# Kernel tuning notes

Hardware: AMD Instinct MI355X
Metric: run time of the kernel (lower is better)

Reference implementation:

```python
import jax, jax.numpy as jnp
import numpy as np

HEAD, DIM, R = 8, 256, 3
RA = (2 * R + 1) ** 2  # 49


def conv2d(x, w, b=None, pad=0, groups=1):
    y = jax.lax.conv_general_dilated(x, w, (1, 1), [(pad, pad), (pad, pad)],
                                     dimension_numbers=('NCHW', 'OIHW', 'NCHW'),
                                     feature_group_count=groups)
    return y if b is None else y + b[None, :, None, None]


def grid_sample(img, grid, mode, padding='zeros'):
    # img [B,C,H,W]; grid [B,Hg,Wg,2] with (x,y) in [-1,1]; align_corners=False.
    B, C, H, W = img.shape
    Hg, Wg = grid.shape[1], grid.shape[2]
    gx = ((grid[..., 0] + 1.0) * W - 1.0) / 2.0
    gy = ((grid[..., 1] + 1.0) * H - 1.0) / 2.0
    if padding == 'border':
        gx = jnp.clip(gx, 0.0, W - 1.0)
        gy = jnp.clip(gy, 0.0, H - 1.0)
    gx = gx.reshape(B, -1)
    gy = gy.reshape(B, -1)

    def gather(iy, ix):
        iyc = jnp.clip(iy, 0, H - 1)
        ixc = jnp.clip(ix, 0, W - 1)
        return jax.vmap(lambda im, a, b: im[:, a, b])(img, iyc, ixc)  # [B,C,N]

    def mask(iy, ix):
        if padding == 'border':
            return jnp.ones(iy.shape, img.dtype)
        return ((ix >= 0) & (ix < W) & (iy >= 0) & (iy < H)).astype(img.dtype)

    if mode == 'nearest':
        ix = jnp.round(gx).astype(jnp.int32)
        iy = jnp.round(gy).astype(jnp.int32)
        out = gather(iy, ix) * mask(iy, ix)[:, None, :]
    else:  # bilinear
        x0f = jnp.floor(gx); y0f = jnp.floor(gy)
        wx = gx - x0f; wy = gy - y0f
        x0 = x0f.astype(jnp.int32); y0 = y0f.astype(jnp.int32)
        out = jnp.zeros((B, C, gx.shape[1]), img.dtype)
        for dx, dy, w in ((0, 0, (1 - wx) * (1 - wy)), (1, 0, wx * (1 - wy)),
                          (0, 1, (1 - wx) * wy), (1, 1, wx * wy)):
            ix = x0 + dx; iy = y0 + dy
            out = out + gather(iy, ix) * (w * mask(iy, ix))[:, None, :]
    return out.reshape(B, C, Hg, Wg)


def mlp2(x, W1, b1, W2, b2):
    return jax.nn.relu(x @ W1.T + b1) @ W2.T + b2


def setup_inputs() -> dict:
    key = jax.random.key(0)
    ks = jax.random.split(key, 32)
    B, H, W, Q = 1, 64, 64, 4096
    f32 = jnp.float32
    rn = lambda k, shp, s=0.02: jax.random.normal(k, shp, f32) * s
    return {
        'inp': jax.random.normal(ks[0], (B, 3, H, W), f32),
        'coord': jax.random.uniform(ks[1], (B, Q, 2), f32, -1.0, 1.0),
        'cell': jnp.full((B, Q, 2), 2.0 / (2 * H), f32),
        'W_enc': rn(ks[2], (64, 3, 3, 3)), 'b_enc': jnp.zeros((64,), f32),
        'W_ch': rn(ks[3], (256, 64, 3, 3)), 'b_ch': jnp.zeros((256,), f32),
        'W_q': rn(ks[4], (256, 256, 3, 3)), 'b_q': jnp.zeros((256,), f32),
        'W_k': rn(ks[5], (256, 256, 3, 3)), 'b_k': jnp.zeros((256,), f32),
        'W_v': rn(ks[6], (256, 256, 3, 3)), 'b_v': jnp.zeros((256,), f32),
        'W_off1': rn(ks[7], (256, 32, 5, 5)), 'b_off1': jnp.zeros((256,), f32),
        'ln_g': jnp.ones((256,), f32), 'ln_b': jnp.zeros((256,), f32),
        'W_off2': rn(ks[8], (98, 256, 1, 1)),
        'Wc1': rn(ks[9], (256, 98)), 'bc1': jnp.zeros((256,), f32),
        'Wc2': rn(ks[10], (49, 256)), 'bc2': jnp.zeros((49,), f32),
        'Wi1': rn(ks[11], (256, 12546)), 'bi1': jnp.zeros((256,), f32),
        'Wi2': rn(ks[12], (3, 256)), 'bi2': jnp.zeros((3,), f32),
        'scale': 2,
    }


def reference(inp, coord, cell, W_enc, b_enc, W_ch, b_ch, W_q, b_q, W_k, b_k,
              W_v, b_v, W_off1, b_off1, ln_g, ln_b, W_off2, Wc1, bc1, Wc2, bc2,
              Wi1, bi1, Wi2, bi2, scale):
    B, _, H, W = inp.shape
    Q = coord.shape[1]
    # gen_feat: encoder stub (conv+relu) -> conv_ch -> q/k/v convs
    feat = conv2d(jax.nn.relu(conv2d(inp, W_enc, b_enc, pad=1)), W_ch, b_ch, pad=1)
    fq = conv2d(feat, W_q, b_q, pad=1)
    fk = conv2d(feat, W_k, b_k, pad=1)
    fv = conv2d(feat, W_v, b_v, pad=1)
    # offset branch: grouped 5x5 conv -> channelwise LN -> GELU -> 1x1 conv (no bias)
    o = conv2d(feat, W_off1, b_off1, pad=2, groups=8)
    oc = o.transpose(0, 2, 3, 1)
    mu = oc.mean(-1, keepdims=True)
    var = ((oc - mu) ** 2).mean(-1, keepdims=True)
    oc = (oc - mu) / jnp.sqrt(var + 1e-5) * ln_g + ln_b
    offsets = conv2d(jax.nn.gelu(oc.transpose(0, 3, 1, 2), approximate=False), W_off2, None, pad=0)  # [B,98,H,W]
    # LR coordinate grid (y,x) at pixel centers in [-1,1]
    ys = -1.0 + 1.0 / H + (2.0 / H) * jnp.arange(H, dtype=inp.dtype)
    xs = -1.0 + 1.0 / W + (2.0 / W) * jnp.arange(W, dtype=inp.dtype)
    coord_lr = jnp.broadcast_to(jnp.stack(jnp.meshgrid(ys, xs, indexing='ij'), 0)[None], (B, 2, H, W))
    sc = coord[:, :, None, :]          # [B,Q,1,2] (y,x)
    g = sc[..., ::-1]                  # (x,y) for grid_sample
    sck = grid_sample(coord_lr, g, 'nearest').transpose(0, 2, 3, 1)  # [B,Q,1,2]
    off = grid_sample(offsets, g, 'nearest').transpose(0, 2, 3, 1).reshape(B, Q, RA, 2)
    off = jnp.tanh(off) * jnp.array([1.0 / (H - 1.0), 1.0 / (W - 1.0)], inp.dtype) * 2.0
    d = jnp.linspace(-R, R, 2 * R + 1).astype(inp.dtype)
    delta = jnp.stack(jnp.meshgrid(d * (2.0 / H), d * (2.0 / W), indexing='ij'), -1).reshape(1, 1, RA, 2)
    sck = sck + delta + off            # [B,Q,49,2] sampling locs (y,x)
    q = grid_sample(fq, g, 'bilinear').transpose(0, 2, 3, 1).reshape(B, Q, HEAD, DIM // HEAD)
    k = grid_sample(fk, sck[..., ::-1], 'nearest').transpose(0, 2, 3, 1).reshape(B, Q, RA, HEAD, DIM // HEAD)
    v = grid_sample(fv, sck[..., ::-1], 'nearest').transpose(0, 2, 3, 1).reshape(B, Q, RA, HEAD, DIM // HEAD)
    attn_val = jnp.einsum('bqhd,bqkhd->bqkh', q, k) / np.sqrt(DIM // HEAD)  # [B,Q,49,8]
    rel = (sc - sck) * jnp.array([H, W], inp.dtype)  # [B,Q,49,2]
    wcoord = mlp2(rel.reshape(B * Q, RA * 2), Wc1, bc1, Wc2, bc2).reshape(B, Q, RA, 1)
    attn = jax.nn.softmax(wcoord + attn_val, axis=2)  # softmax over 49 samples
    feat_in = (v * attn[..., None]).reshape(B, Q, RA * DIM)
    rel_cell = cell * jnp.array([H, W], inp.dtype)
    feat_in = jnp.concatenate([feat_in, rel_cell], -1)  # [B,Q,12546]
    pred = mlp2(feat_in.reshape(B * Q, -1), Wi1, bi1, Wi2, bi2).reshape(B, Q, 3)
    skip = grid_sample(inp, g, 'bilinear', 'border')[:, :, :, 0].transpose(0, 2, 1)
    return pred + skip
```

## Files before the change

kernel.cpp:

```cpp
#include <hip/hip_runtime.h>
#include <hip/hip_bf16.h>


typedef unsigned short u16;
typedef unsigned int u32;
using frag_ab = __attribute__((ext_vector_type(8))) short;
using frag_cd = __attribute__((ext_vector_type(4))) float;

#define HW 4096
#define NQ 4096
#define KBIG 12576
#define SPLITK 16
#define KCHUNK 800
#define KQ 2304
#define QSPLIT 3
#define QCHUNK 768
#define NBLK_QKV (64 * 6 * QSPLIT)
#define NBLK_OFF1 (64 * 8)

static __device__ __forceinline__ u16 f2b(float f) {
  union { __hip_bfloat16 h; u16 u; } c; c.h = __float2bfloat16(f); return c.u;
}
static __device__ __forceinline__ float b2f(u16 v) {
  return __uint_as_float((u32)v << 16);
}
static __device__ __forceinline__ u32 pk2(float a, float b) {
  union { __hip_bfloat162 h; u32 u; } c;
  c.h = __float22bfloat162_rn(float2{a, b});
  return c.u;
}
static __device__ __forceinline__ void glds16(const u16* g, u16* l) {
  __builtin_amdgcn_global_load_lds(
      (const __attribute__((address_space(1))) u32*)(g),
      (__attribute__((address_space(3))) u32*)(l), 16, 0, 0);
}

#define BM 64
#define BN 64
#define BK 32
#define LDSS 40

__global__ __launch_bounds__(256)
void gemm_bt(const u16* __restrict__ A, const u16* __restrict__ Bt,
             void* __restrict__ Cv, const float* __restrict__ bias,
             int N, int K, int ldc, int flags,
             long sA, long sB, long sC, int sBias)
{
  __shared__ u16 As[BM * LDSS];
  __shared__ u16 Bs[BN * LDSS];
  const int z = blockIdx.z;
  A  += (long)z * sA;
  Bt += (long)z * sB;
  const float* bz = bias ? bias + (long)z * sBias : nullptr;

  const int tid  = threadIdx.x;
  const int m0   = blockIdx.x * BM;
  const int n0   = blockIdx.y * BN;
  const int wave = tid >> 6, lane = tid & 63;
  const int mw = (wave & 1) * 32, nw = (wave >> 1) * 32;
  const int lr = lane & 15, lk = lane >> 4;
  const int srow = tid >> 2, scol = (tid & 3) * 8;

  frag_cd acc[2][2] = {};
  const u16* aptr = A + (size_t)(m0 + srow) * K + scol;
  const bool bok  = (n0 + srow) < N;
  const u16* bptr = Bt + (size_t)(n0 + srow) * K + scol;

  uint4 av = *(const uint4*)(aptr);
  uint4 bv = bok ? *(const uint4*)(bptr) : uint4{0u, 0u, 0u, 0u};

  for (int k0 = 0; k0 < K; k0 += BK) {
    *(uint4*)&As[srow * LDSS + scol] = av;
    *(uint4*)&Bs[srow * LDSS + scol] = bv;
    __syncthreads();
    if (k0 + BK < K) {
      av = *(const uint4*)(aptr + k0 + BK);
      bv = bok ? *(const uint4*)(bptr + k0 + BK) : uint4{0u, 0u, 0u, 0u};
    }
    frag_ab af0 = *(const frag_ab*)&As[(mw      + lr) * LDSS + lk * 8];
    frag_ab af1 = *(const frag_ab*)&As[(mw + 16 + lr) * LDSS + lk * 8];
    frag_ab bf0 = *(const frag_ab*)&Bs[(nw      + lr) * LDSS + lk * 8];
    frag_ab bf1 = *(const frag_ab*)&Bs[(nw + 16 + lr) * LDSS + lk * 8];
    acc[0][0] = __builtin_amdgcn_mfma_f32_16x16x32_bf16(af0, bf0, acc[0][0], 0, 0, 0);
    acc[0][1] = __builtin_amdgcn_mfma_f32_16x16x32_bf16(af0, bf1, acc[0][1], 0, 0, 0);
    acc[1][0] = __builtin_amdgcn_mfma_f32_16x16x32_bf16(af1, bf0, acc[1][0], 0, 0, 0);
    acc[1][1] = __builtin_amdgcn_mfma_f32_16x16x32_bf16(af1, bf1, acc[1][1], 0, 0, 0);
    __syncthreads();
  }

  const bool relu = flags & 1;
  const bool obf  = flags & 2;
  #pragma unroll
  for (int i = 0; i < 2; i++)
    #pragma unroll
    for (int j = 0; j < 2; j++) {
      int col = n0 + nw + j * 16 + lr;
      if (col >= N) continue;
      float badd = bz ? bz[col] : 0.f;
      #pragma unroll
      for (int r = 0; r < 4; r++) {
        int row = m0 + mw + i * 16 + lk * 4 + r;
        float v = acc[i][j][r] + badd;
        if (relu) v = fmaxf(v, 0.f);
        size_t idx = (size_t)z * sC + (size_t)row * ldc + col;
        if (obf) ((u16*)Cv)[idx] = f2b(v);
        else     ((float*)Cv)[idx] = v;
      }
    }
}

template<int W3, int SH, int PAD>
__global__ __launch_bounds__(256)
void gemm_conv(const u16* __restrict__ feat, const u16* __restrict__ Bt,
               void* __restrict__ Cv, const float* __restrict__ bias,
               int N, int K, int ldc, int flags, int FC, int cbStride,
               long sB, long sC, int sBias)
{
  __shared__ u16 As[BM * LDSS];
  __shared__ u16 Bs[BN * LDSS];
  const int z = blockIdx.z;
  Bt += (long)z * sB;
  const float* bz = bias ? bias + (long)z * sBias : nullptr;
  const int cb = z * cbStride;

  const int tid  = threadIdx.x;
  const int m0   = blockIdx.x * BM;
  const int n0   = blockIdx.y * BN;
  const int wave = tid >> 6, lane = tid & 63;
  const int mw = (wave & 1) * 32, nw = (wave >> 1) * 32;
  const int lr = lane & 15, lk = lane >> 4;
  const int srow = tid >> 2, scol = (tid & 3) * 8;
  const int p = m0 + srow, y = p >> 6, x = p & 63;

  frag_cd acc[2][2] = {};
  const bool bok  = (n0 + srow) < N;
  const u16* bptr = Bt + (size_t)(n0 + srow) * K + scol;

  auto stageA = [&](int k0) -> uint4 {
    int k = k0 + scol;
    int s = k >> SH;
    int c = k & ((1 << SH) - 1);
    int dy = s / W3, dx = s - dy * W3;
    int yy = y + dy - PAD, xx = x + dx - PAD;
    if (((unsigned)yy < 64u) && ((unsigned)xx < 64u))
      return *(const uint4*)&feat[(size_t)(yy * 64 + xx) * FC + cb + c];
    return uint4{0u, 0u, 0u, 0u};
  };

  uint4 av = stageA(0);
  uint4 bv = bok ? *(const uint4*)(bptr) : uint4{0u, 0u, 0u, 0u};

  for (int k0 = 0; k0 < K; k0 += BK) {
    *(uint4*)&As[srow * LDSS + scol] = av;
    *(uint4*)&Bs[srow * LDSS + scol] = bv;
    __syncthreads();
    if (k0 + BK < K) {
      av = stageA(k0 + BK);
      bv = bok ? *(const uint4*)(bptr + k0 + BK) : uint4{0u, 0u, 0u, 0u};
    }
    frag_ab af0 = *(const frag_ab*)&As[(mw      + lr) * LDSS + lk * 8];
    frag_ab af1 = *(const frag_ab*)&As[(mw + 16 + lr) * LDSS + lk * 8];
    frag_ab bf0 = *(const frag_ab*)&Bs[(nw      + lr) * LDSS + lk * 8];
    frag_ab bf1 = *(const frag_ab*)&Bs[(nw + 16 + lr) * LDSS + lk * 8];
    acc[0][0] = __builtin_amdgcn_mfma_f32_16x16x32_bf16(af0, bf0, acc[0][0], 0, 0, 0);
    acc[0][1] = __builtin_amdgcn_mfma_f32_16x16x32_bf16(af0, bf1, acc[0][1], 0, 0, 0);
    acc[1][0] = __builtin_amdgcn_mfma_f32_16x16x32_bf16(af1, bf0, acc[1][0], 0, 0, 0);
    acc[1][1] = __builtin_amdgcn_mfma_f32_16x16x32_bf16(af1, bf1, acc[1][1], 0, 0, 0);
    __syncthreads();
  }

  const bool relu = flags & 1;
  const bool obf  = flags & 2;
  #pragma unroll
  for (int i = 0; i < 2; i++)
    #pragma unroll
    for (int j = 0; j < 2; j++) {
      int col = n0 + nw + j * 16 + lr;
      if (col >= N) continue;
      float badd = bz ? bz[col] : 0.f;
      #pragma unroll
      for (int r = 0; r < 4; r++) {
        int row = m0 + mw + i * 16 + lk * 4 + r;
        float v = acc[i][j][r] + badd;
        if (relu) v = fmaxf(v, 0.f);
        size_t idx = (size_t)z * sC + (size_t)row * ldc + col;
        if (obf) ((u16*)Cv)[idx] = f2b(v);
        else     ((float*)Cv)[idx] = v;
      }
    }
}

__global__ __launch_bounds__(256)
void gemm_feat(const u16* __restrict__ feat, const u16* __restrict__ Btqkv,
               u16* __restrict__ Pq, const u16* __restrict__ Btoff1,
               float* __restrict__ obuf, const float* __restrict__ b_off1)
{
  __shared__ u16 smem[6656];
  const int bid = blockIdx.x;
  const int tid = threadIdx.x;
  const int wave = tid >> 6, lane = tid & 63;
  const int lr = lane & 15, lk = lane >> 4;

  if (bid < NBLK_QKV) {
    u16* As = smem;
    u16* Bs = smem + 64 * 40;
    const int mz  = bid & 63;
    const int rest = bid >> 6;
    const int ny  = rest % 6;
    const int z   = rest / 6;
    const int m0  = mz * 64;
    const int n0  = ny * 128;
    const int kbeg = z * QCHUNK;
    const int kend = kbeg + QCHUNK;
    const int nw = wave * 32;
    const int arow = tid >> 2, acol = (tid & 3) * 8;
    const int p = m0 + arow, y = p >> 6, x = p & 63;

    frag_cd acc[4][2] = {};
    const u16* bbase = Btqkv + (size_t)(n0 + (tid >> 2)) * KQ + (tid & 3) * 8 + kbeg;
    u16* bdst = &Bs[(size_t)tid * 8];

    auto stageA = [&](int k0) -> uint4 {
      int k = k0 + acol;
      int s = k >> 8, c = k & 255;
      int dy = s / 3, dx = s - dy * 3;
      int yy = y + dy - 1, xx = x + dx - 1;
      if (((unsigned)yy < 64u) && ((unsigned)xx < 64u))
        return *(const uint4*)&feat[(size_t)(yy * 64 + xx) * 256 + c];
      return uint4{0u, 0u, 0u, 0u};
    };

    uint4 av = stageA(kbeg);

    for (int k0 = kbeg; k0 < kend; k0 += BK) {
      glds16(bbase + (k0 - kbeg), bdst);
      glds16(bbase + (k0 - kbeg) + (size_t)64 * KQ, bdst + 2048);
      *(uint4*)&As[arow * LDSS + acol] = av;
      __syncthreads();
      if (k0 + BK < kend) av = stageA(k0 + BK);
      frag_ab af[4];
      #pragma unroll
      for (int i = 0; i < 4; i++)
        af[i] = *(const frag_ab*)&As[(i * 16 + lr) * LDSS + lk * 8];
      #pragma unroll
      for (int j = 0; j < 2; j++) {
        frag_ab bf = *(const frag_ab*)&Bs[(nw + j * 16 + lr) * 32 + lk * 8];
        #pragma unroll
        for (int i = 0; i < 4; i++)
          acc[i][j] = __builtin_amdgcn_mfma_f32_16x16x32_bf16(af[i], bf, acc[i][j], 0, 0, 0);
      }
      __syncthreads();
    }

    #pragma unroll
    for (int i = 0; i < 4; i++)
      #pragma unroll
      for (int j = 0; j < 2; j++) {
        int col = n0 + nw + j * 16 + lr;
        #pragma unroll
        for (int r = 0; r < 4; r++) {
          int row = m0 + i * 16 + lk * 4 + r;
          Pq[(size_t)z * (NQ * 768) + (size_t)row * 768 + col] = f2b(acc[i][j][r]);
        }
      }
  } else {
    u16* As = smem;
    u16* Bs = smem + 64 * 40;
    const int t  = bid - NBLK_QKV;
    const int m0 = (t & 63) * 64;
    const int g  = t >> 6;
    const int cb = g * 32;
    const u16* Bt = Btoff1 + (size_t)g * 32 * 800;
    const float* bz = b_off1 + g * 32;
    const int mw = (wave & 1) * 32, nw = (wave >> 1) * 32;
    const int srow = tid >> 2, scol = (tid & 3) * 8;
    const int p = m0 + srow, y = p >> 6, x = p & 63;

    frag_cd acc[2][2] = {};
    const bool bok  = srow < 32;
    const u16* bptr = Bt + (size_t)srow * 800 + scol;

    auto stageA = [&](int k0) -> uint4 {
      int k = k0 + scol;
      int s = k >> 5;
      int c = k & 31;
      int dy = s / 5, dx = s - dy * 5;
      int yy = y + dy - 2, xx = x + dx - 2;
      if (((unsigned)yy < 64u) && ((unsigned)xx < 64u))
        return *(const uint4*)&feat[(size_t)(yy * 64 + xx) * 256 + cb + c];
      return uint4{0u, 0u, 0u, 0u};
    };

    uint4 av = stageA(0);
    uint4 bv = bok ? *(const uint4*)(bptr) : uint4{0u, 0u, 0u, 0u};

    for (int k0 = 0; k0 < 800; k0 += BK) {
      *(uint4*)&As[srow * LDSS + scol] = av;
      *(uint4*)&Bs[srow * LDSS + scol] = bv;
      __syncthreads();
      if (k0 + BK < 800) {
        av = stageA(k0 + BK);
        bv = bok ? *(const uint4*)(bptr + k0 + BK) : uint4{0u, 0u, 0u, 0u};
      }
      frag_ab af0 = *(const frag_ab*)&As[(mw      + lr) * LDSS + lk * 8];
      frag_ab af1 = *(const frag_ab*)&As[(mw + 16 + lr) * LDSS + lk * 8];
      frag_ab bf0 = *(const frag_ab*)&Bs[(nw      + lr) * LDSS + lk * 8];
      frag_ab bf1 = *(const frag_ab*)&Bs[(nw + 16 + lr) * LDSS + lk * 8];
      acc[0][0] = __builtin_amdgcn_mfma_f32_16x16x32_bf16(af0, bf0, acc[0][0], 0, 0, 0);
      acc[0][1] = __builtin_amdgcn_mfma_f32_16x16x32_bf16(af0, bf1, acc[0][1], 0, 0, 0);
      acc[1][0] = __builtin_amdgcn_mfma_f32_16x16x32_bf16(af1, bf0, acc[1][0], 0, 0, 0);
      acc[1][1] = __builtin_amdgcn_mfma_f32_16x16x32_bf16(af1, bf1, acc[1][1], 0, 0, 0);
      __syncthreads();
    }

    #pragma unroll
    for (int i = 0; i < 2; i++)
      #pragma unroll
      for (int j = 0; j < 2; j++) {
        int col = nw + j * 16 + lr;
        if (col >= 32) continue;
        float badd = bz[col];
        #pragma unroll
        for (int r = 0; r < 4; r++) {
          int row = m0 + mw + i * 16 + lk * 4 + r;
          obuf[(size_t)row * 256 + g * 32 + col] = acc[i][j][r] + badd;
        }
      }
  }
}

__global__ __launch_bounds__(256)
void reduce_qkv(const u16* __restrict__ P, const float* __restrict__ bias,
                u16* __restrict__ outb, float* __restrict__ outV)
{
  int i8 = blockIdx.x * 256 + threadIdx.x;
  if (i8 >= NQ * 96) return;
  size_t i = (size_t)i8 * 8;
  int row = (int)(i / 768);
  int c = (int)(i % 768);
  float v[8];
  #pragma unroll
  for (int t = 0; t < 8; t++) v[t] = bias[c + t];
  for (int z = 0; z < QSPLIT; z++) {
    uint4 a = *(const uint4*)&P[(size_t)z * (NQ * 768) + i];
    u32 aw[4] = {a.x, a.y, a.z, a.w};
    #pragma unroll
    for (int t = 0; t < 4; t++) {
      v[2 * t]     += __uint_as_float(aw[t] << 16);
      v[2 * t + 1] += __uint_as_float(aw[t] & 0xffff0000u);
    }
  }
  uint4 ob = {pk2(v[0], v[1]), pk2(v[2], v[3]), pk2(v[4], v[5]), pk2(v[6], v[7])};
  *(uint4*)&outb[i] = ob;
  if (c >= 512) {
    float* dst = outV + (size_t)row * 256 + (c - 512);
    *(float4*)dst       = float4{v[0], v[1], v[2], v[3]};
    *(float4*)(dst + 4) = float4{v[4], v[5], v[6], v[7]};
  }
}

__global__ __launch_bounds__(512, 4)
void gemm_big(const u16* __restrict__ Bt, const float* __restrict__ fqkvV,
              const float* __restrict__ attnval, const int* __restrict__ vidx,
              const float* __restrict__ cell, u16* __restrict__ P)
{
  __shared__ u16 As[128 * LDSS];
  __shared__ u16 Bs[256 * 32];
  __shared__ int   s_vidx[5 * 128];
  __shared__ float s_attn[5 * 128 * 8];
  const int tid  = threadIdx.x;
  const int m0   = blockIdx.x * 128;
  const int z    = blockIdx.y;
  const int kbeg = z * KCHUNK;
  const int kend = min(KBIG, kbeg + KCHUNK);
  const int jbeg = kbeg >> 8;
  const int jcnt = ((kend - 1) >> 8) - jbeg + 1;
  const int wave = tid >> 6, lane = tid & 63;
  const int mw = (wave & 1) * 64, nwv = (wave >> 1) * 64;
  const int lr = lane & 15, lk = lane >> 4;
  const int arow = tid >> 2, acol = (tid & 3) * 8;
  const int q = m0 + arow;

  for (int t = tid; t < 128 * jcnt; t += 512) {
    int r = t & 127, jj = t >> 7;
    int j = jbeg + jj;
    s_vidx[t] = (j < 49) ? vidx[(m0 + r) * 49 + j] : -1;
  }
  for (int t = tid; t < 128 * 8 * jcnt; t += 512) {
    int h = t & 7, rr = (t >> 3) & 127, jj = t >> 10;
    int j = jbeg + jj;
    s_attn[t] = (j < 49) ? attnval[((size_t)((m0 + rr) * 49 + j)) * 8 + h] : 0.f;
  }
  __syncthreads();

  auto loadA = [&](int k0, float4& f0, float4& f1, float& w) {
    const int k = k0 + acol;
    const int j = k >> 8, c = k & 255;
    f0 = float4{0.f, 0.f, 0.f, 0.f};
    f1 = float4{0.f, 0.f, 0.f, 0.f};
    w = 0.f;
    if (j < 49) {
      const int jj = j - jbeg;
      int id = s_vidx[jj * 128 + arow];
      if (id >= 0) {
        w = s_attn[(jj * 128 + arow) * 8 + (c >> 5)];
        const float* src = fqkvV + (size_t)id * 256 + c;
        f0 = *(const float4*)src;
        f1 = *(const float4*)(src + 4);
      }
    } else if (c == 0) {
      f0.x = cell[q * 2]; f0.y = cell[q * 2 + 1];
      w = 64.f;
    }
  };

  frag_cd acc[4][4] = {};
  float4 f0c, f1c; float wc_;
  loadA(kbeg, f0c, f1c, wc_);
  const u16* bbase = Bt + (size_t)(tid >> 2) * KBIG + (tid & 3) * 8 + kbeg;
  u16* bdst = &Bs[(size_t)tid * 8];

  for (int k0 = kbeg; k0 < kend; k0 += BK) {
    glds16(bbase + (k0 - kbeg), bdst);
    glds16(bbase + (k0 - kbeg) + (size_t)128 * KBIG, bdst + 4096);
    {
      uint4 av;
      av.x = pk2(f0c.x * wc_, f0c.y * wc_);
      av.y = pk2(f0c.z * wc_, f0c.w * wc_);
      av.z = pk2(f1c.x * wc_, f1c.y * wc_);
      av.w = pk2(f1c.z * wc_, f1c.w * wc_);
      *(uint4*)&As[arow * LDSS + acol] = av;
    }
    __syncthreads();
    if (k0 + BK < kend) loadA(k0 + BK, f0c, f1c, wc_);
    frag_ab af[4];
    #pragma unroll
    for (int i = 0; i < 4; i++)
      af[i] = *(const frag_ab*)&As[(mw + i * 16 + lr) * LDSS + lk * 8];
    #pragma unroll
    for (int j = 0; j < 4; j++) {
      frag_ab bf = *(const frag_ab*)&Bs[(nwv + j * 16 + lr) * 32 + lk * 8];
      #pragma unroll
      for (int i = 0; i < 4; i++)
        acc[i][j] = __builtin_amdgcn_mfma_f32_16x16x32_bf16(af[i], bf, acc[i][j], 0, 0, 0);
    }
    __syncthreads();
  }

  #pragma unroll
  for (int i = 0; i < 4; i++)
    #pragma unroll
    for (int j = 0; j < 4; j++) {
      int col = nwv + j * 16 + lr;
      #pragma unroll
      for (int r = 0; r < 4; r++) {
        int row = m0 + mw + i * 16 + lk * 4 + r;
        P[(size_t)z * (NQ * 256) + (size_t)row * 256 + col] = f2b(acc[i][j][r]);
      }
    }
}

__global__ __launch_bounds__(256)
void reduce_final(const u16* __restrict__ Pb, const float* __restrict__ bi1,
                  const float* __restrict__ Wi2, const float* __restrict__ bi2,
                  const float* __restrict__ skipb, float* __restrict__ out)
{
  const int q = blockIdx.x, c = threadIdx.x;
  float s = 0.f;
  #pragma unroll
  for (int z = 0; z < SPLITK; z++)
    s += b2f(Pb[(size_t)z * (NQ * 256) + (size_t)q * 256 + c]);
  s += bi1[c];
  s = fmaxf(s, 0.f);

  __shared__ float part[3][4];
  float p0 = s * Wi2[c], p1 = s * Wi2[256 + c], p2 = s * Wi2[512 + c];
  #pragma unroll
  for (int off = 32; off; off >>= 1) {
    p0 += __shfl_xor(p0, off);
    p1 += __shfl_xor(p1, off);
    p2 += __shfl_xor(p2, off);
  }
  if ((c & 63) == 0) {
    int w = c >> 6;
    part[0][w] = p0; part[1][w] = p1; part[2][w] = p2;
  }
  __syncthreads();
  if (c < 3)
    out[q * 3 + c] = bi2[c] + skipb[q * 3 + c]
                   + part[c][0] + part[c][1] + part[c][2] + part[c][3];
}

__global__ __launch_bounds__(512)
void softmax_k(const float* __restrict__ wc, float* __restrict__ attnval)
{
  const int q = blockIdx.x;
  const int tid = threadIdx.x;
  const int hh = tid >> 6, l = tid & 63;
  float v = (l < 49) ? wc[(size_t)q * 49 + l] + attnval[((size_t)q * 49 + l) * 8 + hh]
                     : -1e30f;
  float m = v;
  #pragma unroll
  for (int off = 32; off; off >>= 1) m = fmaxf(m, __shfl_xor(m, off));
  float e = (l < 49) ? expf(v - m) : 0.f;
  float s = e;
  #pragma unroll
  for (int off = 32; off; off >>= 1) s += __shfl_xor(s, off);
  if (l < 49) attnval[((size_t)q * 49 + l) * 8 + hh] = e / s;
}

static __device__ __forceinline__
void packconv(const float* __restrict__ W, u16* __restrict__ Bt,
              int Cin, int K2, int idx)
{
  int o  = idx / (Cin * K2);
  int r  = idx - o * (Cin * K2);
  int ci = r / K2;
  int s  = r - ci * K2;
  Bt[(size_t)o * (Cin * K2) + s * Cin + ci] = f2b(W[idx]);
}
static __device__ __forceinline__
void packcast(const float* __restrict__ W, u16* __restrict__ Bt,
              int Kin, int Kout, int idx)
{
  int n = idx / Kout, k = idx - n * Kout;
  Bt[idx] = f2b(k < Kin ? W[(size_t)n * Kin + k] : 0.f);
}

#define SZ_CH   147456
#define SZ_QKV  589824
#define SZ_OFF1 204800
#define SZ_OFF2 25088
#define SZ_C1   32768
#define SZ_C2   12544
#define SZ_WI1  3219456
#define SZ_PACK (SZ_CH + 3*SZ_QKV + SZ_OFF1 + SZ_OFF2 + SZ_C1 + SZ_C2 + 768 + SZ_WI1)

__global__ void pack_all(const float* W_ch, const float* W_q, const float* W_k,
                         const float* W_v, const float* W_off1, const float* W_off2,
                         const float* Wc1, const float* Wc2, const float* Wi1,
                         const float* b_q, const float* b_k, const float* b_v,
                         u16* Btch, u16* Btqkv, u16* Btoff1, u16* Btoff2,
                         u16* Btc1, u16* Btc2, u16* Wi1p, float* bqkv)
{
  int i = blockIdx.x * 256 + threadIdx.x;
  if (i < SZ_CH) { packconv(W_ch, Btch, 64, 9, i); return; }
  i -= SZ_CH;
  if (i < SZ_QKV) { packconv(W_q, Btqkv, 256, 9, i); return; }
  i -= SZ_QKV;
  if (i < SZ_QKV) { packconv(W_k, Btqkv + (size_t)256 * 2304, 256, 9, i); return; }
  i -= SZ_QKV;
  if (i < SZ_QKV) { packconv(W_v, Btqkv + (size_t)512 * 2304, 256, 9, i); return; }
  i -= SZ_QKV;
  if (i < SZ_OFF1) { packconv(W_off1, Btoff1, 32, 25, i); return; }
  i -= SZ_OFF1;
  if (i < SZ_OFF2) { packcast(W_off2, Btoff2, 256, 256, i); return; }
  i -= SZ_OFF2;
  if (i < SZ_C1) { packcast(Wc1, Btc1, 98, 128, i); return; }
  i -= SZ_C1;
  if (i < SZ_C2) { packcast(Wc2, Btc2, 256, 256, i); return; }
  i -= SZ_C2;
  if (i < 768) {
    bqkv[i] = (i < 256) ? b_q[i] : (i < 512) ? b_k[i - 256] : b_v[i - 512];
    return;
  }
  i -= 768;
  if (i < SZ_WI1) { packcast(Wi1, Wi1p, 12546, 12576, i); }
}

__global__ __launch_bounds__(64)
void conv_enc(const float* __restrict__ inp, const float* __restrict__ W,
              const float* __restrict__ b, u16* __restrict__ feat1)
{
  const int p = blockIdx.x, c = threadIdx.x;
  const int y = p >> 6, x = p & 63;
  float s = b[c];
  #pragma unroll
  for (int ci = 0; ci < 3; ci++)
    #pragma unroll
    for (int dy = 0; dy < 3; dy++) {
      int yy = y + dy - 1;
      if ((unsigned)yy >= 64u) continue;
      #pragma unroll
      for (int dx = 0; dx < 3; dx++) {
        int xx = x + dx - 1;
        if ((unsigned)xx >= 64u) continue;
        s += inp[ci * HW + yy * 64 + xx] * W[((c * 3 + ci) * 3 + dy) * 3 + dx];
      }
    }
  feat1[(size_t)p * 64 + c] = f2b(fmaxf(s, 0.f));
}

__global__ __launch_bounds__(256)
void ln_gelu(const float* __restrict__ x, const float* __restrict__ g,
             const float* __restrict__ b, u16* __restrict__ y)
{
  const int p = blockIdx.x, c = threadIdx.x;
  __shared__ float r1[4], r2[4];
  float v = x[(size_t)p * 256 + c];
  float s1 = v, s2 = v * v;
  #pragma unroll
  for (int off = 32; off; off >>= 1) {
    s1 += __shfl_xor(s1, off);
    s2 += __shfl_xor(s2, off);
  }
  if ((c & 63) == 0) { r1[c >> 6] = s1; r2[c >> 6] = s2; }
  __syncthreads();
  float t1 = r1[0] + r1[1] + r1[2] + r1[3];
  float t2 = r2[0] + r2[1] + r2[2] + r2[3];
  float mu  = t1 * (1.f / 256.f);
  float var = t2 * (1.f / 256.f) - mu * mu;
  float xn = (v - mu) * rsqrtf(var + 1e-5f) * g[c] + b[c];
  float ge = 0.5f * xn * (1.f + erff(xn * 0.70710678118654752f));
  y[(size_t)p * 256 + c] = f2b(ge);
}

__global__ __launch_bounds__(256)
void sampler(const float* __restrict__ coord, const u16* __restrict__ fqkvb,
             const float* __restrict__ offs, const float* __restrict__ inp,
             float* __restrict__ attnval, u16* __restrict__ relbuf,
             int* __restrict__ vidx, float* __restrict__ skipb)
{
  const int q = blockIdx.x;
  const int tid = threadIdx.x;
  __shared__ float s_off[98];
  __shared__ int s_idx[49];
  __shared__ float s_q[256];

  const float c0 = coord[q * 2], c1 = coord[q * 2 + 1];
  const float gxp = ((c1 + 1.f) * 64.f - 1.f) * 0.5f;
  const float gyp = ((c0 + 1.f) * 64.f - 1.f) * 0.5f;
  const int ixn = (int)rintf(gxp), iyn = (int)rintf(gyp);
  const bool inn = ((unsigned)ixn < 64u) && ((unsigned)iyn < 64u);

  if (tid < 98) {
    float v = inn ? offs[(size_t)(iyn * 64 + ixn) * 98 + tid] : 0.f;
    s_off[tid] = tanhf(v) * (2.f / 63.f);
  }
  __syncthreads();

  const float scky = inn ? (-1.f + (float)(2 * iyn + 1) * (1.f / 64.f)) : 0.f;
  const float sckx = inn ? (-1.f + (float)(2 * ixn + 1) * (1.f / 64.f)) : 0.f;

  if (tid < 49) {
    const int a = tid / 7, bb = tid - a * 7;
    float sy = scky + (float)(a - 3) * (2.f / 64.f) + s_off[2 * tid];
    float sx = sckx + (float)(bb - 3) * (2.f / 64.f) + s_off[2 * tid + 1];
    relbuf[(size_t)q * 128 + 2 * tid]     = f2b((c0 - sy) * 64.f);
    relbuf[(size_t)q * 128 + 2 * tid + 1] = f2b((c1 - sx) * 64.f);
    float gx2 = ((sx + 1.f) * 64.f - 1.f) * 0.5f;
    float gy2 = ((sy + 1.f) * 64.f - 1.f) * 0.5f;
    int ix2 = (int)rintf(gx2), iy2 = (int)rintf(gy2);
    int id = (((unsigned)ix2 < 64u) && ((unsigned)iy2 < 64u)) ? (iy2 * 64 + ix2) : -1;
    s_idx[tid] = id;
    vidx[q * 49 + tid] = id;
  } else if (tid >= 98 && tid < 128) {
    relbuf[(size_t)q * 128 + tid] = 0;
  }

  {
    const float x0f = floorf(gxp), y0f = floorf(gyp);
    const float wx = gxp - x0f, wy = gyp - y0f;
    const int x0 = (int)x0f, y0 = (int)y0f;
    float qc = 0.f;
    #pragma unroll
    for (int t = 0; t < 4; t++) {
      int xi = x0 + (t & 1), yi = y0 + (t >> 1);
      if (((unsigned)xi < 64u) && ((unsigned)yi < 64u)) {
        float w = ((t & 1) ? wx : 1.f - wx) * ((t >> 1) ? wy : 1.f - wy);
        qc += w * b2f(fqkvb[(size_t)(yi * 64 + xi) * 768 + tid]);
      }
    }
    s_q[tid] = qc * 0.17677669529663687f;
  }

  if (tid < 3) {
    float gx = fminf(fmaxf(gxp, 0.f), 63.f);
    float gy = fminf(fmaxf(gyp, 0.f), 63.f);
    float xf = floorf(gx), yf = floorf(gy);
    float wxs = gx - xf, wys = gy - yf;
    int xa = (int)xf, ya = (int)yf;
    int xb = min(xa + 1, 63), yb = min(ya + 1, 63);
    const float* ch = inp + tid * HW;
    float v = (1.f - wxs) * (1.f - wys) * ch[ya * 64 + xa]
            + wxs * (1.f - wys) * ch[ya * 64 + xb]
            + (1.f - wxs) * wys * ch[yb * 64 + xa]
            + wxs * wys * ch[yb * 64 + xb];
    skipb[q * 3 + tid] = v;
  }
  __syncthreads();

  const int wave = tid >> 6, lane = tid & 63;
  const int half = lane >> 5, sub = lane & 31;
  const int ch0 = sub * 8;
  const int h = sub >> 2;
  float qv[8];
  #pragma unroll
  for (int i = 0; i < 8; i++) qv[i] = s_q[ch0 + i];

  for (int it = 0; it < 7; it++) {
    int j = it * 8 + wave * 2 + half;
    if (j >= 49) break;
    int id = s_idx[j];
    float p = 0.f;
    if (id >= 0) {
      uint4 kv = *(const uint4*)&fqkvb[(size_t)id * 768 + 256 + ch0];
      u32 w0 = kv.x, w1 = kv.y, w2 = kv.z, w3 = kv.w;
      p = fmaf(qv[0], __uint_as_float(w0 << 16), p);
      p = fmaf(qv[1], __uint_as_float(w0 & 0xffff0000u), p);
      p = fmaf(qv[2], __uint_as_float(w1 << 16), p);
      p = fmaf(qv[3], __uint_as_float(w1 & 0xffff0000u), p);
      p = fmaf(qv[4], __uint_as_float(w2 << 16), p);
      p = fmaf(qv[5], __uint_as_float(w2 & 0xffff0000u), p);
      p = fmaf(qv[6], __uint_as_float(w3 << 16), p);
      p = fmaf(qv[7], __uint_as_float(w3 & 0xffff0000u), p);
    }
    p += __shfl_down(p, 2, 4);
    p += __shfl_down(p, 1, 4);
    if ((sub & 3) == 0) attnval[((size_t)q * 49 + j) * 8 + h] = p;
  }
}

extern "C" void kernel_launch(void* const* d_in, const int* in_sizes, int n_in,
                              void* d_out, int out_size, void* d_ws, size_t ws_size,
                              hipStream_t stream)
{
  const float* inp    = (const float*)d_in[0];
  const float* coord  = (const float*)d_in[1];
  const float* cell   = (const float*)d_in[2];
  const float* W_enc  = (const float*)d_in[3];
  const float* b_enc  = (const float*)d_in[4];
  const float* W_ch   = (const float*)d_in[5];
  const float* b_ch   = (const float*)d_in[6];
  const float* W_q    = (const float*)d_in[7];
  const float* b_q    = (const float*)d_in[8];
  const float* W_k    = (const float*)d_in[9];
  const float* b_k    = (const float*)d_in[10];
  const float* W_v    = (const float*)d_in[11];
  const float* b_v    = (const float*)d_in[12];
  const float* W_off1 = (const float*)d_in[13];
  const float* b_off1 = (const float*)d_in[14];
  const float* ln_g   = (const float*)d_in[15];
  const float* ln_b   = (const float*)d_in[16];
  const float* W_off2 = (const float*)d_in[17];
  const float* Wc1    = (const float*)d_in[18];
  const float* bc1    = (const float*)d_in[19];
  const float* Wc2    = (const float*)d_in[20];
  const float* bc2    = (const float*)d_in[21];
  const float* Wi1    = (const float*)d_in[22];
  const float* bi1    = (const float*)d_in[23];
  const float* Wi2    = (const float*)d_in[24];
  const float* bi2    = (const float*)d_in[25];

  char* base = (char*)d_ws;
  size_t off = 0;
  auto alloc = [&](size_t bytes) -> char* {
    char* r = base + off;
    off = (off + bytes + 255) & ~(size_t)255;
    return r;
  };

  float* obuf   = (float*)alloc((size_t)HW * 256 * 4);
  u16*   ocg    = (u16*)  alloc((size_t)HW * 256 * 2);
  float* offsb  = (float*)alloc((size_t)HW * 98 * 4);
  u16*   feat1  = (u16*)  alloc((size_t)HW * 64 * 2);
  u16*   feat   = (u16*)  alloc((size_t)HW * 256 * 2);
  u16*   hid1   = (u16*)  alloc((size_t)NQ * 256 * 2);
  float* wcb    = (float*)alloc((size_t)NQ * 49 * 4);
  u16*   relbuf = (u16*)  alloc((size_t)NQ * 128 * 2);
  u16*   Btqkv  = (u16*)  alloc((size_t)768 * 2304 * 2);
  u16*   Btch   = (u16*)  alloc((size_t)256 * 576 * 2);
  u16*   Btoff1 = (u16*)  alloc((size_t)256 * 800 * 2);
  u16*   Btoff2 = (u16*)  alloc((size_t)98 * 256 * 2);
  u16*   Btc1   = (u16*)  alloc((size_t)256 * 128 * 2);
  u16*   Btc2   = (u16*)  alloc((size_t)49 * 256 * 2);
  u16* Pb = (u16*)base;
  u16* Pqb = (u16*)(base + ((size_t)36 << 20));
  {
    size_t need = ((size_t)36 << 20) + (size_t)QSPLIT * NQ * 768 * 2;
    if (off < need) off = (need + 255) & ~(size_t)255;
  }
  u16*   fqkvb   = (u16*)  alloc((size_t)HW * 768 * 2);
  float* fqkvV   = (float*)alloc((size_t)HW * 256 * 4);
  float* attnval = (float*)alloc((size_t)NQ * 49 * 8 * 4);
  int*   vidxb   = (int*)  alloc((size_t)NQ * 49 * 4);
  float* skipb   = (float*)alloc((size_t)NQ * 3 * 4);
  u16*   Wi1p    = (u16*)  alloc((size_t)256 * KBIG * 2);
  float* bqkv    = (float*)alloc(768 * 4);
  (void)ws_size; (void)in_sizes; (void)n_in; (void)out_size;

  pack_all<<<(SZ_PACK + 255) / 256, 256, 0, stream>>>(
      W_ch, W_q, W_k, W_v, W_off1, W_off2, Wc1, Wc2, Wi1, b_q, b_k, b_v,
      Btch, Btqkv, Btoff1, Btoff2, Btc1, Btc2, Wi1p, bqkv);

  conv_enc<<<HW, 64, 0, stream>>>(inp, W_enc, b_enc, feat1);
  gemm_conv<3, 6, 1><<<dim3(64, 4, 1), 256, 0, stream>>>(
      feat1, Btch, feat, b_ch, 256, 576, 256, 2, 64, 0, 0, 0, 0);
  gemm_feat<<<NBLK_QKV + NBLK_OFF1, 256, 0, stream>>>(
      feat, Btqkv, Pqb, Btoff1, obuf, b_off1);
  reduce_qkv<<<(NQ * 96 + 255) / 256, 256, 0, stream>>>(Pqb, bqkv, fqkvb, fqkvV);
  ln_gelu<<<HW, 256, 0, stream>>>(obuf, ln_g, ln_b, ocg);
  gemm_bt<<<dim3(64, 2, 1), 256, 0, stream>>>(ocg, Btoff2, offsb, nullptr,
      98, 256, 98, 0, 0, 0, 0, 0);

  sampler<<<NQ, 256, 0, stream>>>(coord, fqkvb, offsb, inp,
                                  attnval, relbuf, vidxb, skipb);
  gemm_bt<<<dim3(64, 4, 1), 256, 0, stream>>>(relbuf, Btc1, hid1, bc1,
      256, 128, 256, 3, 0, 0, 0, 0);
  gemm_bt<<<dim3(64, 1, 1), 256, 0, stream>>>(hid1, Btc2, wcb, bc2,
      49, 256, 49, 0, 0, 0, 0, 0);
  softmax_k<<<NQ, 512, 0, stream>>>(wcb, attnval);

  gemm_big<<<dim3(32, SPLITK), 512, 0, stream>>>(
      Wi1p, fqkvV, attnval, vidxb, cell, Pb);
  reduce_final<<<NQ, 256, 0, stream>>>(Pb, bi1, Wi2, bi2, skipb, (float*)d_out);
}
```

Measured before the change: 288.5 us.

## Store V features in bf16 for gathers and retune big GEMM split-K

reduce_qkv now writes the V slice as packed bf16 instead of fp32. gemm_big gathers 16-byte bf16 rows and unpacks them before scaling by the attention weight, which halves the bytes moved by the irregular V gather. The big GEMM also goes from 16 to 24 split-K slices with a smaller K chunk. The shared index and attention staging arrays shrink to 3 j-slots and launch bounds ask for 6 blocks per CU, aiming for more parallelism and occupancy. The cost is an extra bf16 rounding of V before the multiply and more partial sums written and reduced.

```diff
diff --git a/kernel.cpp b/kernel.cpp
--- a/kernel.cpp
+++ b/kernel.cpp
@@ -10,8 +10,9 @@
 #define HW 4096
 #define NQ 4096
 #define KBIG 12576
-#define SPLITK 16
-#define KCHUNK 800
+#define SPLITK 24
+#define KCHUNK 544
+#define JMAX 3
 #define KQ 2304
 #define QSPLIT 3
 #define QCHUNK 768
@@ -331,7 +332,7 @@
 
 __global__ __launch_bounds__(256)
 void reduce_qkv(const u16* __restrict__ P, const float* __restrict__ bias,
-                u16* __restrict__ outb, float* __restrict__ outV)
+                u16* __restrict__ outb, u16* __restrict__ outV)
 {
   int i8 = blockIdx.x * 256 + threadIdx.x;
   if (i8 >= NQ * 96) return;
@@ -353,21 +354,19 @@
   uint4 ob = {pk2(v[0], v[1]), pk2(v[2], v[3]), pk2(v[4], v[5]), pk2(v[6], v[7])};
   *(uint4*)&outb[i] = ob;
   if (c >= 512) {
-    float* dst = outV + (size_t)row * 256 + (c - 512);
-    *(float4*)dst       = float4{v[0], v[1], v[2], v[3]};
-    *(float4*)(dst + 4) = float4{v[4], v[5], v[6], v[7]};
-  }
-}
-
-__global__ __launch_bounds__(512, 4)
-void gemm_big(const u16* __restrict__ Bt, const float* __restrict__ fqkvV,
+    *(uint4*)&outV[(size_t)row * 256 + (c - 512)] = ob;
+  }
+}
+
+__global__ __launch_bounds__(512, 6)
+void gemm_big(const u16* __restrict__ Bt, const u16* __restrict__ fqkvV,
               const float* __restrict__ attnval, const int* __restrict__ vidx,
               const float* __restrict__ cell, u16* __restrict__ P)
 {
   __shared__ u16 As[128 * LDSS];
   __shared__ u16 Bs[256 * 32];
-  __shared__ int   s_vidx[5 * 128];
-  __shared__ float s_attn[5 * 128 * 8];
+  __shared__ int   s_vidx[JMAX * 128];
+  __shared__ float s_attn[JMAX * 128 * 8];
   const int tid  = threadIdx.x;
   const int m0   = blockIdx.x * 128;
   const int z    = blockIdx.y;
@@ -393,30 +392,27 @@
   }
   __syncthreads();
 
-  auto loadA = [&](int k0, float4& f0, float4& f1, float& w) {
+  auto loadA = [&](int k0, uint4& kv, float& w) {
     const int k = k0 + acol;
     const int j = k >> 8, c = k & 255;
-    f0 = float4{0.f, 0.f, 0.f, 0.f};
-    f1 = float4{0.f, 0.f, 0.f, 0.f};
+    kv = uint4{0u, 0u, 0u, 0u};
     w = 0.f;
     if (j < 49) {
       const int jj = j - jbeg;
       int id = s_vidx[jj * 128 + arow];
       if (id >= 0) {
         w = s_attn[(jj * 128 + arow) * 8 + (c >> 5)];
-        const float* src = fqkvV + (size_t)id * 256 + c;
-        f0 = *(const float4*)src;
-        f1 = *(const float4*)(src + 4);
+        kv = *(const uint4*)(fqkvV + (size_t)id * 256 + c);
       }
     } else if (c == 0) {
-      f0.x = cell[q * 2]; f0.y = cell[q * 2 + 1];
+      kv.x = pk2(cell[q * 2], cell[q * 2 + 1]);
       w = 64.f;
     }
   };
 
   frag_cd acc[4][4] = {};
-  float4 f0c, f1c; float wc_;
-  loadA(kbeg, f0c, f1c, wc_);
+  uint4 kvc; float wc_;
+  loadA(kbeg, kvc, wc_);
   const u16* bbase = Bt + (size_t)(tid >> 2) * KBIG + (tid & 3) * 8 + kbeg;
   u16* bdst = &Bs[(size_t)tid * 8];
 
@@ -424,15 +420,20 @@
     glds16(bbase + (k0 - kbeg), bdst);
     glds16(bbase + (k0 - kbeg) + (size_t)128 * KBIG, bdst + 4096);
     {
+      u32 aw[4] = {kvc.x, kvc.y, kvc.z, kvc.w};
       uint4 av;
-      av.x = pk2(f0c.x * wc_, f0c.y * wc_);
-      av.y = pk2(f0c.z * wc_, f0c.w * wc_);
-      av.z = pk2(f1c.x * wc_, f1c.y * wc_);
-      av.w = pk2(f1c.z * wc_, f1c.w * wc_);
+      u32 avw[4];
+      #pragma unroll
+      for (int t = 0; t < 4; t++) {
+        float lo = __uint_as_float(aw[t] << 16) * wc_;
+        float hi = __uint_as_float(aw[t] & 0xffff0000u) * wc_;
+        avw[t] = pk2(lo, hi);
+      }
+      av.x = avw[0]; av.y = avw[1]; av.z = avw[2]; av.w = avw[3];
       *(uint4*)&As[arow * LDSS + acol] = av;
     }
     __syncthreads();
-    if (k0 + BK < kend) loadA(k0 + BK, f0c, f1c, wc_);
+    if (k0 + BK < kend) loadA(k0 + BK, kvc, wc_);
     frag_ab af[4];
     #pragma unroll
     for (int i = 0; i < 4; i++)
@@ -781,7 +782,7 @@
     if (off < need) off = (need + 255) & ~(size_t)255;
   }
   u16*   fqkvb   = (u16*)  alloc((size_t)HW * 768 * 2);
-  float* fqkvV   = (float*)alloc((size_t)HW * 256 * 4);
+  u16*   fqkvVb  = (u16*)  alloc((size_t)HW * 256 * 2);
   float* attnval = (float*)alloc((size_t)NQ * 49 * 8 * 4);
   int*   vidxb   = (int*)  alloc((size_t)NQ * 49 * 4);
   float* skipb   = (float*)alloc((size_t)NQ * 3 * 4);
@@ -798,7 +799,7 @@
       feat1, Btch, feat, b_ch, 256, 576, 256, 2, 64, 0, 0, 0, 0);
   gemm_feat<<<NBLK_QKV + NBLK_OFF1, 256, 0, stream>>>(
       feat, Btqkv, Pqb, Btoff1, obuf, b_off1);
-  reduce_qkv<<<(NQ * 96 + 255) / 256, 256, 0, stream>>>(Pqb, bqkv, fqkvb, fqkvV);
+  reduce_qkv<<<(NQ * 96 + 255) / 256, 256, 0, stream>>>(Pqb, bqkv, fqkvb, fqkvVb);
   ln_gelu<<<HW, 256, 0, stream>>>(obuf, ln_g, ln_b, ocg);
   gemm_bt<<<dim3(64, 2, 1), 256, 0, stream>>>(ocg, Btoff2, offsb, nullptr,
       98, 256, 98, 0, 0, 0, 0, 0);
@@ -812,6 +813,6 @@
   softmax_k<<<NQ, 512, 0, stream>>>(wcb, attnval);
 
   gemm_big<<<dim3(32, SPLITK), 512, 0, stream>>>(
-      Wi1p, fqkvV, attnval, vidxb, cell, Pb);
+      Wi1p, fqkvVb, attnval, vidxb, cell, Pb);
   reduce_final<<<NQ, 256, 0, stream>>>(Pb, bi1, Wi2, bi2, skipb, (float*)d_out);
 }
```

New measurement: 455.2 us. 1.58x slower.
